# Kernel tuning notes

Measured on AMD Instinct MI355X. Metric: run time of the kernel, lower is better.

Reference implementation:

```python
import jax, jax.numpy as jnp
import numpy as np

CODEBOOK_SIZE = 8192
CODEBOOK_DIM = 1024
HIDDEN_DIM = 4096
OUT_DIM = 1024
B, M = 32, 576


def setup_inputs() -> dict:
    key = jax.random.key(0)
    k_idx, k_cb, k_w1, k_w2 = jax.random.split(key, 4)
    index = jax.random.randint(k_idx, (B, M), 0, CODEBOOK_SIZE, dtype=jnp.int32)
    # codebook initialized as sqrt(d) * randn, as in the torch module
    codebook = (CODEBOOK_DIM ** 0.5) * jax.random.normal(k_cb, (CODEBOOK_SIZE, CODEBOOK_DIM), dtype=jnp.float32)
    s1 = 1.0 / np.sqrt(CODEBOOK_DIM)
    s2 = 1.0 / np.sqrt(HIDDEN_DIM)
    W1 = s1 * jax.random.normal(k_w1, (CODEBOOK_DIM, HIDDEN_DIM), dtype=jnp.float32)
    b1 = jnp.zeros((HIDDEN_DIM,), dtype=jnp.float32)
    W2 = s2 * jax.random.normal(k_w2, (HIDDEN_DIM, OUT_DIM), dtype=jnp.float32)
    b2 = jnp.zeros((OUT_DIM,), dtype=jnp.float32)
    return {"index": index, "codebook": codebook, "W1": W1, "b1": b1, "W2": W2, "b2": b2}


def reference(index, codebook, W1, b1, W2, b2):
    # one_hot(index) @ codebook is mathematically an index gather:
    # quantized[b, m, :] = codebook[index[b, m], :]
    quantized = jnp.take(codebook, index, axis=0)  # [B, M, D]
    # Decoder_ff: 2-layer GELU MLP (D -> 4D -> D)
    h = jax.nn.gelu(jnp.einsum('bmd,dh->bmh', quantized, W1) + b1)
    rec = jnp.einsum('bmh,ho->bmo', h, W2) + b2
    return rec
```

## Files before the change

kernel.cpp:

```cpp
#include <hip/hip_runtime.h>
#include <stdint.h>

typedef __attribute__((ext_vector_type(8))) short s16x8;
typedef __attribute__((ext_vector_type(4))) float f32x4;

__device__ __forceinline__ short f2bf(float x) {
  uint32_t u = __builtin_bit_cast(uint32_t, x);
  u += 0x7FFFu + ((u >> 16) & 1u);
  return (short)(u >> 16);
}

__device__ __forceinline__ void gload16(void* l, const void* g) {
  __builtin_amdgcn_global_load_lds(
      (const __attribute__((address_space(1))) void*)g,
      (__attribute__((address_space(3))) void*)l, 16, 0, 0);
}

__device__ __forceinline__ float gelu_tanh(float x) {
  float u = 0.7978845608028654f * (x + 0.044715f * x * x * x);
  float e = __expf(2.0f * u);
  return x - x / (e + 1.0f);
}

__global__ void gather_cvt(const float* __restrict__ cb, const int* __restrict__ idx,
                           short* __restrict__ out) {
  int m = blockIdx.x * 2 + (threadIdx.x >> 7);
  int c = (threadIdx.x & 127) * 8;
  const float* s = cb + (size_t)idx[m] * 1024 + c;
  s16x8 o;
#pragma unroll
  for (int j = 0; j < 8; ++j) o[j] = f2bf(s[j]);
  *(s16x8*)(out + (size_t)m * 1024 + c) = o;
}

__global__ void cvt_T(const float* __restrict__ in, short* __restrict__ out, int K, int N) {
  int Kb = K >> 3;
  int t = blockIdx.x * 256 + threadIdx.x;
  if (t >= N * Kb) return;
  int n = t / Kb;
  int k8 = (t - n * Kb) * 8;
  const float* s = in + (size_t)k8 * N + n;
  s16x8 o;
#pragma unroll
  for (int j = 0; j < 8; ++j) o[j] = f2bf(s[(size_t)j * N]);
  *(s16x8*)(out + (size_t)n * K + k8) = o;
}

template <int MODE, int K, int N>
__global__ __launch_bounds__(512, 2) void gemm8p(
    const short* __restrict__ A, const short* __restrict__ Bt,
    const float* __restrict__ bias, void* __restrict__ Cv) {
  constexpr int BM = 288, BN = 256;
  constexpr int ATS = BM * 64;
  constexpr int LDSH = (BM + BN) * 64;
  __shared__ short lds[2 * LDSH + 2048];

  constexpr int NBN = N / BN;
  const int nwg = gridDim.x;
  int swz = blockIdx.x;
  swz = (swz & 7) * (nwg >> 3) + (swz >> 3);
  const int bm = swz / NBN, bn = swz - (swz / NBN) * NBN;

  const int tid = threadIdx.x;
  const int wid = tid >> 6, lane = tid & 63;
  const int wr = wid >> 2, wc = wid & 3;
  const int lr = lane & 15, hi = lane >> 4;

  const int sl = (tid & 7) ^ ((tid >> 3) & 7);
  const long rstep = (long)64 * K;
  const short* aptr0 = A + (long)(bm * BM + (tid >> 3)) * K + sl * 8;
  const short* aptr4 = A + (long)(bm * BM + 256 + ((tid >> 3) & 31)) * K + sl * 8;
  const short* bptr0 = Bt + (long)(bn * BN + (tid >> 3)) * K + sl * 8;
  const int wlds = wid * 512;
  const int a4rel = (wid < 4) ? (16384 + wid * 512) : -1;

  const int aRB = (wr * 144 + lr) * 64;
  const int bRB = ATS + (wc * 64 + lr) * 64;
  const int sk0 = ((0 + hi) ^ (lr & 7)) * 8;
  const int sk1 = ((4 + hi) ^ (lr & 7)) * 8;

  f32x4 acc[9][4] = {};
  s16x8 af[5][2], bf[2][2][2];

  constexpr int NT = K >> 6;

#pragma unroll
  for (int r = 0; r < 4; ++r) gload16(&lds[ATS + r * 4096 + wlds], bptr0 + r * rstep);
  gload16(&lds[0 * 4096 + wlds], aptr0 + 0 * rstep);
  gload16(&lds[2 * 4096 + wlds], aptr0 + 2 * rstep);
  gload16(&lds[3 * 4096 + wlds], aptr0 + 3 * rstep);
  gload16(&lds[1 * 4096 + wlds], aptr0 + 1 * rstep);
  gload16((a4rel >= 0) ? &lds[a4rel] : &lds[2 * LDSH + (wid & 3) * 512], aptr4);
  asm volatile("s_waitcnt vmcnt(2)" ::: "memory");
  __builtin_amdgcn_s_barrier();

  for (int t = 0; t < NT; ++t) {
    const int cb = (t & 1) * LDSH;
    const int nb = LDSH - cb;
    const int kt = ((t + 1 < NT) ? (t + 1) : 0) << 6;

#pragma unroll
    for (int mi = 0; mi < 4; ++mi) {
      af[mi][0] = *(const s16x8*)&lds[cb + aRB + mi * 1024 + sk0];
      af[mi][1] = *(const s16x8*)&lds[cb + aRB + mi * 1024 + sk1];
    }
#pragma unroll
    for (int ni = 0; ni < 2; ++ni) {
      bf[0][ni][0] = *(const s16x8*)&lds[cb + bRB + ni * 1024 + sk0];
      bf[0][ni][1] = *(const s16x8*)&lds[cb + bRB + ni * 1024 + sk1];
    }
    gload16(&lds[nb + ATS + 0 * 4096 + wlds], bptr0 + 0 * rstep + kt);
    gload16(&lds[nb + ATS + 1 * 4096 + wlds], bptr0 + 1 * rstep + kt);
    __builtin_amdgcn_s_barrier();
    asm volatile("s_waitcnt lgkmcnt(0)" ::: "memory");
    __builtin_amdgcn_s_setprio(1);
#pragma unroll
    for (int mi = 0; mi < 4; ++mi)
#pragma unroll
      for (int ni = 0; ni < 2; ++ni)
#pragma unroll
        for (int ks = 0; ks < 2; ++ks)
          acc[mi][ni] = __builtin_amdgcn_mfma_f32_16x16x32_bf16(af[mi][ks], bf[0][ni][ks], acc[mi][ni], 0, 0, 0);
    __builtin_amdgcn_s_setprio(0);
    __builtin_amdgcn_s_barrier();

#pragma unroll
    for (int ni = 0; ni < 2; ++ni) {
      bf[1][ni][0] = *(const s16x8*)&lds[cb + bRB + (2 + ni) * 1024 + sk0];
      bf[1][ni][1] = *(const s16x8*)&lds[cb + bRB + (2 + ni) * 1024 + sk1];
    }
    gload16(&lds[nb + ATS + 2 * 4096 + wlds], bptr0 + 2 * rstep + kt);
    gload16(&lds[nb + ATS + 3 * 4096 + wlds], bptr0 + 3 * rstep + kt);
    __builtin_amdgcn_s_barrier();
    asm volatile("s_waitcnt lgkmcnt(0)" ::: "memory");
    __builtin_amdgcn_s_setprio(1);
#pragma unroll
    for (int mi = 0; mi < 4; ++mi)
#pragma unroll
      for (int ni = 0; ni < 2; ++ni)
#pragma unroll
        for (int ks = 0; ks < 2; ++ks)
          acc[mi][2 + ni] = __builtin_amdgcn_mfma_f32_16x16x32_bf16(af[mi][ks], bf[1][ni][ks], acc[mi][2 + ni], 0, 0, 0);
    __builtin_amdgcn_s_setprio(0);
    asm volatile("s_waitcnt vmcnt(4)" ::: "memory");
    __builtin_amdgcn_s_barrier();

#pragma unroll
    for (int mi = 0; mi < 5; ++mi) {
      af[mi][0] = *(const s16x8*)&lds[cb + aRB + (4 + mi) * 1024 + sk0];
      af[mi][1] = *(const s16x8*)&lds[cb + aRB + (4 + mi) * 1024 + sk1];
    }
    gload16(&lds[nb + 0 * 4096 + wlds], aptr0 + 0 * rstep + kt);
    gload16(&lds[nb + 2 * 4096 + wlds], aptr0 + 2 * rstep + kt);
    gload16(&lds[nb + 3 * 4096 + wlds], aptr0 + 3 * rstep + kt);
    __builtin_amdgcn_s_barrier();
    asm volatile("s_waitcnt lgkmcnt(0)" ::: "memory");
    __builtin_amdgcn_s_setprio(1);
#pragma unroll
    for (int mi = 0; mi < 5; ++mi)
#pragma unroll
      for (int ni = 0; ni < 2; ++ni)
#pragma unroll
        for (int ks = 0; ks < 2; ++ks)
          acc[4 + mi][ni] = __builtin_amdgcn_mfma_f32_16x16x32_bf16(af[mi][ks], bf[0][ni][ks], acc[4 + mi][ni], 0, 0, 0);
    __builtin_amdgcn_s_setprio(0);
    __builtin_amdgcn_s_barrier();

    gload16(&lds[nb + 1 * 4096 + wlds], aptr0 + 1 * rstep + kt);
    gload16((a4rel >= 0) ? &lds[nb + a4rel] : &lds[2 * LDSH + (wid & 3) * 512], aptr4 + kt);
    __builtin_amdgcn_s_barrier();
    __builtin_amdgcn_s_setprio(1);
#pragma unroll
    for (int mi = 0; mi < 5; ++mi)
#pragma unroll
      for (int ni = 0; ni < 2; ++ni)
#pragma unroll
        for (int ks = 0; ks < 2; ++ks)
          acc[4 + mi][2 + ni] = __builtin_amdgcn_mfma_f32_16x16x32_bf16(af[mi][ks], bf[1][ni][ks], acc[4 + mi][2 + ni], 0, 0, 0);
    __builtin_amdgcn_s_setprio(0);
    asm volatile("s_waitcnt vmcnt(2)" ::: "memory");
    __builtin_amdgcn_s_barrier();
  }

  const int m0 = bm * BM + wr * 144 + hi * 4;
  const int n0 = bn * BN + wc * 64 + lr;
#pragma unroll
  for (int j = 0; j < 4; ++j) {
    const int n = n0 + j * 16;
    const float bv = bias[n];
#pragma unroll
    for (int i = 0; i < 9; ++i) {
      f32x4 v = acc[i][j];
#pragma unroll
      for (int r = 0; r < 4; ++r) {
        const int m = m0 + i * 16 + r;
        float x = v[r] + bv;
        if (MODE == 1) {
          ((short*)Cv)[(size_t)m * N + n] = f2bf(gelu_tanh(x));
        } else {
          ((float*)Cv)[(size_t)m * N + n] = x;
        }
      }
    }
  }
}

extern "C" void kernel_launch(void* const* d_in, const int* in_sizes, int n_in,
                              void* d_out, int out_size, void* d_ws, size_t ws_size,
                              hipStream_t stream) {
  const int* idx = (const int*)d_in[0];
  const float* cb = (const float*)d_in[1];
  const float* W1 = (const float*)d_in[2];
  const float* b1 = (const float*)d_in[3];
  const float* W2 = (const float*)d_in[4];
  const float* b2 = (const float*)d_in[5];
  float* out = (float*)d_out;

  const int Mtot = 32 * 576;

  char* ws = (char*)d_ws;
  short* aq = (short*)(ws);
  short* w1t = (short*)(ws + (size_t)40 * 1024 * 1024);
  short* w2t = (short*)(ws + (size_t)48 * 1024 * 1024);
  short* h = (short*)(ws + (size_t)56 * 1024 * 1024);

  gather_cvt<<<Mtot / 2, 256, 0, stream>>>(cb, idx, aq);
  cvt_T<<<2048, 256, 0, stream>>>(W1, w1t, 1024, 4096);
  cvt_T<<<2048, 256, 0, stream>>>(W2, w2t, 4096, 1024);

  size_t avail = (ws_size > (size_t)56 * 1024 * 1024) ? ws_size - (size_t)56 * 1024 * 1024 : 0;
  int nc = 1;
  while (nc < 8 && (size_t)(Mtot / nc) * 8192 > avail) nc <<= 1;
  const int Mc = Mtot / nc;

  for (int c = 0; c < nc; ++c) {
    gemm8p<1, 1024, 4096><<<(Mc / 288) * 16, 512, 0, stream>>>(
        aq + (size_t)c * Mc * 1024, w1t, b1, (void*)h);
    gemm8p<2, 4096, 1024><<<(Mc / 288) * 4, 512, 0, stream>>>(
        h, w2t, b2, (void*)(out + (size_t)c * Mc * 1024));
  }
}
```

Before: 395.9 us.

## Shrink GEMM block tile to 144x256 with 1x8 wave layout

Halves the M block tile from 288 to 144 and rearranges the 8 waves into one row of 8 columns, each wave owning a 144x32 output slice. The K-loop drops from four phases to two, and A loading is restructured into two full row chunks plus a 16-row partial chunk. This doubles the workgroup count and cuts per-wave accumulators, aiming at better occupancy and wave balance. In exchange each block reuses loaded data less, which raises global and LDS traffic per FLOP.

```diff
diff --git a/kernel.cpp b/kernel.cpp
--- a/kernel.cpp
+++ b/kernel.cpp
@@ -47,13 +47,13 @@
 }
 
 template <int MODE, int K, int N>
-__global__ __launch_bounds__(512, 2) void gemm8p(
+__global__ __launch_bounds__(512, 2) void gemm2p(
     const short* __restrict__ A, const short* __restrict__ Bt,
     const float* __restrict__ bias, void* __restrict__ Cv) {
-  constexpr int BM = 288, BN = 256;
+  constexpr int BM = 144, BN = 256;
   constexpr int ATS = BM * 64;
   constexpr int LDSH = (BM + BN) * 64;
-  __shared__ short lds[2 * LDSH + 2048];
+  __shared__ short lds[2 * LDSH + 512];
 
   constexpr int NBN = N / BN;
   const int nwg = gridDim.x;
@@ -63,34 +63,30 @@
 
   const int tid = threadIdx.x;
   const int wid = tid >> 6, lane = tid & 63;
-  const int wr = wid >> 2, wc = wid & 3;
   const int lr = lane & 15, hi = lane >> 4;
 
   const int sl = (tid & 7) ^ ((tid >> 3) & 7);
   const long rstep = (long)64 * K;
   const short* aptr0 = A + (long)(bm * BM + (tid >> 3)) * K + sl * 8;
-  const short* aptr4 = A + (long)(bm * BM + 256 + ((tid >> 3) & 31)) * K + sl * 8;
+  const short* aptrP = A + (long)(bm * BM + 128 + ((tid >> 3) & 15)) * K + sl * 8;
   const short* bptr0 = Bt + (long)(bn * BN + (tid >> 3)) * K + sl * 8;
   const int wlds = wid * 512;
-  const int a4rel = (wid < 4) ? (16384 + wid * 512) : -1;
-
-  const int aRB = (wr * 144 + lr) * 64;
-  const int bRB = ATS + (wc * 64 + lr) * 64;
-  const int sk0 = ((0 + hi) ^ (lr & 7)) * 8;
+
+  const int aRB = lr * 64;
+  const int bRB = ATS + (wid * 32 + lr) * 64;
+  const int sk0 = (hi ^ (lr & 7)) * 8;
   const int sk1 = ((4 + hi) ^ (lr & 7)) * 8;
 
-  f32x4 acc[9][4] = {};
-  s16x8 af[5][2], bf[2][2][2];
+  f32x4 acc[9][2] = {};
+  s16x8 af[5][2], bf[2][2];
 
   constexpr int NT = K >> 6;
 
 #pragma unroll
   for (int r = 0; r < 4; ++r) gload16(&lds[ATS + r * 4096 + wlds], bptr0 + r * rstep);
-  gload16(&lds[0 * 4096 + wlds], aptr0 + 0 * rstep);
-  gload16(&lds[2 * 4096 + wlds], aptr0 + 2 * rstep);
-  gload16(&lds[3 * 4096 + wlds], aptr0 + 3 * rstep);
-  gload16(&lds[1 * 4096 + wlds], aptr0 + 1 * rstep);
-  gload16((a4rel >= 0) ? &lds[a4rel] : &lds[2 * LDSH + (wid & 3) * 512], aptr4);
+  gload16(&lds[0 + wlds], aptr0);
+  gload16(&lds[4096 + wlds], aptr0 + rstep);
+  gload16((wid < 2) ? &lds[8192 + wlds] : &lds[2 * LDSH], aptrP);
   asm volatile("s_waitcnt vmcnt(2)" ::: "memory");
   __builtin_amdgcn_s_barrier();
 
@@ -105,42 +101,23 @@
       af[mi][1] = *(const s16x8*)&lds[cb + aRB + mi * 1024 + sk1];
     }
 #pragma unroll
-    for (int ni = 0; ni < 2; ++ni) {
-      bf[0][ni][0] = *(const s16x8*)&lds[cb + bRB + ni * 1024 + sk0];
-      bf[0][ni][1] = *(const s16x8*)&lds[cb + bRB + ni * 1024 + sk1];
-    }
-    gload16(&lds[nb + ATS + 0 * 4096 + wlds], bptr0 + 0 * rstep + kt);
-    gload16(&lds[nb + ATS + 1 * 4096 + wlds], bptr0 + 1 * rstep + kt);
+    for (int nj = 0; nj < 2; ++nj) {
+      bf[nj][0] = *(const s16x8*)&lds[cb + bRB + nj * 1024 + sk0];
+      bf[nj][1] = *(const s16x8*)&lds[cb + bRB + nj * 1024 + sk1];
+    }
+#pragma unroll
+    for (int r = 0; r < 4; ++r)
+      gload16(&lds[nb + ATS + r * 4096 + wlds], bptr0 + r * rstep + kt);
     __builtin_amdgcn_s_barrier();
     asm volatile("s_waitcnt lgkmcnt(0)" ::: "memory");
     __builtin_amdgcn_s_setprio(1);
 #pragma unroll
     for (int mi = 0; mi < 4; ++mi)
 #pragma unroll
-      for (int ni = 0; ni < 2; ++ni)
+      for (int nj = 0; nj < 2; ++nj)
 #pragma unroll
         for (int ks = 0; ks < 2; ++ks)
-          acc[mi][ni] = __builtin_amdgcn_mfma_f32_16x16x32_bf16(af[mi][ks], bf[0][ni][ks], acc[mi][ni], 0, 0, 0);
-    __builtin_amdgcn_s_setprio(0);
-    __builtin_amdgcn_s_barrier();
-
-#pragma unroll
-    for (int ni = 0; ni < 2; ++ni) {
-      bf[1][ni][0] = *(const s16x8*)&lds[cb + bRB + (2 + ni) * 1024 + sk0];
-      bf[1][ni][1] = *(const s16x8*)&lds[cb + bRB + (2 + ni) * 1024 + sk1];
-    }
-    gload16(&lds[nb + ATS + 2 * 4096 + wlds], bptr0 + 2 * rstep + kt);
-    gload16(&lds[nb + ATS + 3 * 4096 + wlds], bptr0 + 3 * rstep + kt);
-    __builtin_amdgcn_s_barrier();
-    asm volatile("s_waitcnt lgkmcnt(0)" ::: "memory");
-    __builtin_amdgcn_s_setprio(1);
-#pragma unroll
-    for (int mi = 0; mi < 4; ++mi)
-#pragma unroll
-      for (int ni = 0; ni < 2; ++ni)
-#pragma unroll
-        for (int ks = 0; ks < 2; ++ks)
-          acc[mi][2 + ni] = __builtin_amdgcn_mfma_f32_16x16x32_bf16(af[mi][ks], bf[1][ni][ks], acc[mi][2 + ni], 0, 0, 0);
+          acc[mi][nj] = __builtin_amdgcn_mfma_f32_16x16x32_bf16(af[mi][ks], bf[nj][ks], acc[mi][nj], 0, 0, 0);
     __builtin_amdgcn_s_setprio(0);
     asm volatile("s_waitcnt vmcnt(4)" ::: "memory");
     __builtin_amdgcn_s_barrier();
@@ -150,50 +127,36 @@
       af[mi][0] = *(const s16x8*)&lds[cb + aRB + (4 + mi) * 1024 + sk0];
       af[mi][1] = *(const s16x8*)&lds[cb + aRB + (4 + mi) * 1024 + sk1];
     }
-    gload16(&lds[nb + 0 * 4096 + wlds], aptr0 + 0 * rstep + kt);
-    gload16(&lds[nb + 2 * 4096 + wlds], aptr0 + 2 * rstep + kt);
-    gload16(&lds[nb + 3 * 4096 + wlds], aptr0 + 3 * rstep + kt);
+    gload16(&lds[nb + 0 + wlds], aptr0 + kt);
+    gload16(&lds[nb + 4096 + wlds], aptr0 + rstep + kt);
+    gload16((wid < 2) ? &lds[nb + 8192 + wlds] : &lds[2 * LDSH], aptrP + kt);
     __builtin_amdgcn_s_barrier();
     asm volatile("s_waitcnt lgkmcnt(0)" ::: "memory");
     __builtin_amdgcn_s_setprio(1);
 #pragma unroll
     for (int mi = 0; mi < 5; ++mi)
 #pragma unroll
-      for (int ni = 0; ni < 2; ++ni)
+      for (int nj = 0; nj < 2; ++nj)
 #pragma unroll
         for (int ks = 0; ks < 2; ++ks)
-          acc[4 + mi][ni] = __builtin_amdgcn_mfma_f32_16x16x32_bf16(af[mi][ks], bf[0][ni][ks], acc[4 + mi][ni], 0, 0, 0);
-    __builtin_amdgcn_s_setprio(0);
-    __builtin_amdgcn_s_barrier();
-
-    gload16(&lds[nb + 1 * 4096 + wlds], aptr0 + 1 * rstep + kt);
-    gload16((a4rel >= 0) ? &lds[nb + a4rel] : &lds[2 * LDSH + (wid & 3) * 512], aptr4 + kt);
-    __builtin_amdgcn_s_barrier();
-    __builtin_amdgcn_s_setprio(1);
-#pragma unroll
-    for (int mi = 0; mi < 5; ++mi)
-#pragma unroll
-      for (int ni = 0; ni < 2; ++ni)
-#pragma unroll
-        for (int ks = 0; ks < 2; ++ks)
-          acc[4 + mi][2 + ni] = __builtin_amdgcn_mfma_f32_16x16x32_bf16(af[mi][ks], bf[1][ni][ks], acc[4 + mi][2 + ni], 0, 0, 0);
+          acc[4 + mi][nj] = __builtin_amdgcn_mfma_f32_16x16x32_bf16(af[mi][ks], bf[nj][ks], acc[4 + mi][nj], 0, 0, 0);
     __builtin_amdgcn_s_setprio(0);
     asm volatile("s_waitcnt vmcnt(2)" ::: "memory");
     __builtin_amdgcn_s_barrier();
   }
 
-  const int m0 = bm * BM + wr * 144 + hi * 4;
-  const int n0 = bn * BN + wc * 64 + lr;
-#pragma unroll
-  for (int j = 0; j < 4; ++j) {
-    const int n = n0 + j * 16;
+  const int m0 = bm * BM + hi * 4;
+  const int n0 = bn * BN + wid * 32 + lr;
+#pragma unroll
+  for (int nj = 0; nj < 2; ++nj) {
+    const int n = n0 + nj * 16;
     const float bv = bias[n];
 #pragma unroll
-    for (int i = 0; i < 9; ++i) {
-      f32x4 v = acc[i][j];
+    for (int mi = 0; mi < 9; ++mi) {
+      f32x4 v = acc[mi][nj];
 #pragma unroll
       for (int r = 0; r < 4; ++r) {
-        const int m = m0 + i * 16 + r;
+        const int m = m0 + mi * 16 + r;
         float x = v[r] + bv;
         if (MODE == 1) {
           ((short*)Cv)[(size_t)m * N + n] = f2bf(gelu_tanh(x));
@@ -234,9 +197,9 @@
   const int Mc = Mtot / nc;
 
   for (int c = 0; c < nc; ++c) {
-    gemm8p<1, 1024, 4096><<<(Mc / 288) * 16, 512, 0, stream>>>(
+    gemm2p<1, 1024, 4096><<<(Mc / 144) * 16, 512, 0, stream>>>(
         aq + (size_t)c * Mc * 1024, w1t, b1, (void*)h);
-    gemm8p<2, 4096, 1024><<<(Mc / 288) * 4, 512, 0, stream>>>(
+    gemm2p<2, 4096, 1024><<<(Mc / 144) * 4, 512, 0, stream>>>(
         h, w2t, b2, (void*)(out + (size_t)c * Mc * 1024));
   }
 }
```

Measured after the change: 475.0 us. +20.0%, slower.
